# Performance work log

Measured on AMD Instinct MI355X. Metric: run time of the kernel, lower is better.

The kernel has to match this reference:

```python
import jax, jax.numpy as jnp
import numpy as np

N, E, IN_DIM, OUT_DIM = 50000, 800000, 128, 128
NEG_SLOPE = 0.01  # F.leaky_relu default


def gcn_conv(x, W, b, src, dst, n_nodes):
    """PyG GCNConv: symmetric norm with self-loops, linear (no bias) -> aggregate -> +bias.
    Self-loop contribution added analytically (norm = deg_inv_sqrt[i]^2) instead of
    materializing an extended edge list."""
    h = x @ W.T  # [N, out]
    deg = jnp.zeros((n_nodes,), x.dtype).at[dst].add(1.0) + 1.0  # in-degree incl. self-loop
    dis = jax.lax.rsqrt(deg)  # deg^{-1/2}
    norm = dis[src] * dis[dst]  # [E]
    msgs = h[src] * norm[:, None]  # gather + scale, [E, out]
    agg = jax.ops.segment_sum(msgs, dst, num_segments=n_nodes)  # scatter-add
    agg = agg + h * (dis * dis)[:, None]  # self-loop messages
    return agg + b


def setup_inputs() -> dict:
    key = jax.random.key(0)
    ks = jax.random.split(key, 6)
    x = jax.random.normal(ks[0], (N, IN_DIM), jnp.float32)
    edge_index = jax.random.randint(ks[1], (2, E), 0, N, dtype=jnp.int32)
    batch = jnp.zeros((N,), jnp.int32)
    W1 = jax.random.normal(ks[2], (OUT_DIM, IN_DIM), jnp.float32) * (1.0 / np.sqrt(IN_DIM))
    b1 = jnp.zeros((OUT_DIM,), jnp.float32)
    W2 = jax.random.normal(ks[3], (OUT_DIM, OUT_DIM), jnp.float32) * (1.0 / np.sqrt(OUT_DIM))
    b2 = jnp.zeros((OUT_DIM,), jnp.float32)
    return {"x": x, "edge_index": edge_index, "batch": batch,
            "W1": W1, "b1": b1, "W2": W2, "b2": b2}


def reference(x, edge_index, batch, W1, b1, W2, b2):
    src, dst = edge_index[0], edge_index[1]
    n = x.shape[0]
    h = gcn_conv(x, W1, b1, src, dst, n)
    h = jax.nn.leaky_relu(h, NEG_SLOPE)
    # dropout is identity in eval mode (training=False)
    return gcn_conv(h, W2, b2, src, dst, n)
```

## Files before the change

### kernel.cpp

```cpp
#include <hip/hip_runtime.h>
#include <hip/hip_bf16.h>
#include <hip/hip_fp16.h>

#define DIM 128
#define NCHUNK 256
#define XLD 136
#define WLD 136

typedef unsigned short u16;
typedef unsigned int u32;
typedef __attribute__((ext_vector_type(8))) short bf16x8;
typedef __attribute__((ext_vector_type(4))) float f32x4;

__device__ __forceinline__ float bfbits2f(u16 u) {
    return __uint_as_float(((u32)u) << 16);
}
__device__ __forceinline__ u16 f2bf(float f) {
    __hip_bfloat16 b = __float2bfloat16(f);
    return *reinterpret_cast<u16*>(&b);
}
__device__ __forceinline__ u32 pack2bf(float lo, float hi) {
    return (u32)f2bf(lo) | ((u32)f2bf(hi) << 16);
}
__device__ __forceinline__ float h16tof(u16 u) {
    __half hh = *reinterpret_cast<__half*>(&u);
    return __half2float(hh);
}
__device__ __forceinline__ u16 ftoh16(float f) {
    __half hh = __float2half(f);
    return *reinterpret_cast<u16*>(&hh);
}

__global__ void k_probe(const u16* __restrict__ x, int* __restrict__ flagp) {
    if (threadIdx.x == 0 && blockIdx.x == 0) {
        int weird = 0;
        for (int i = 0; i < 256; i += 2) {
            u16 v = x[i];
            int e = (v >> 7) & 0xff;
            if ((v & 0x7fff) != 0 && (e >= 133 || e <= 100)) weird++;
        }
        *flagp = (weird > 16) ? 1 : 0;
    }
}

__global__ __launch_bounds__(256) void k_count(const int* __restrict__ dst,
                                               int* __restrict__ counts,
                                               int* __restrict__ rank, int E) {
    int e = blockIdx.x * blockDim.x + threadIdx.x;
    if (e < E) rank[e] = atomicAdd(&counts[dst[e]], 1);
}

__global__ __launch_bounds__(256) void k_chunksum(const int* __restrict__ counts,
                                                  int* __restrict__ chunksum,
                                                  int N, int chunk) {
    __shared__ int r[256];
    int t = threadIdx.x, b = blockIdx.x;
    int idx = b * chunk + t;
    r[t] = (t < chunk && idx < N) ? counts[idx] : 0;
    __syncthreads();
    for (int off = 128; off > 0; off >>= 1) {
        if (t < off) r[t] += r[t + off];
        __syncthreads();
    }
    if (t == 0) chunksum[b] = r[0];
}

__global__ void k_scanbase(const int* __restrict__ chunksum,
                           int* __restrict__ chunkbase,
                           int* __restrict__ rowptr, int N) {
    if (threadIdx.x == 0 && blockIdx.x == 0) {
        int run = 0;
        for (int i = 0; i < NCHUNK; ++i) { chunkbase[i] = run; run += chunksum[i]; }
        rowptr[N] = run;
    }
}

__global__ __launch_bounds__(256) void k_rowptr(const int* __restrict__ counts,
                                                const int* __restrict__ chunkbase,
                                                int* __restrict__ rowptr,
                                                float* __restrict__ dis,
                                                u32* __restrict__ pay,
                                                int N, int chunk) {
    __shared__ int sc[256];
    int t = threadIdx.x, b = blockIdx.x;
    int idx = b * chunk + t;
    int v = (t < chunk && idx < N) ? counts[idx] : 0;
    sc[t] = v;
    __syncthreads();
    for (int off = 1; off < 256; off <<= 1) {
        int add = (t >= off) ? sc[t - off] : 0;
        __syncthreads();
        sc[t] += add;
        __syncthreads();
    }
    if (t < chunk && idx < N) {
        rowptr[idx] = chunkbase[b] + sc[t] - v;
        float dv = rsqrtf((float)v + 1.0f);
        dis[idx] = dv;
        pay[idx] = ((u32)idx << 16) | (u32)ftoh16(dv);
    }
}

__global__ __launch_bounds__(256) void k_fill(const int* __restrict__ src,
                                              const int* __restrict__ dst,
                                              const int* __restrict__ rowptr,
                                              const int* __restrict__ rank,
                                              const u32* __restrict__ pay,
                                              u32* __restrict__ elist, int E) {
    int e = blockIdx.x * blockDim.x + threadIdx.x;
    if (e < E) {
        int d = dst[e];
        int s = src[e];
        elist[rowptr[d] + rank[e]] = pay[s];
    }
}

__global__ __launch_bounds__(256) void k_gemm(const void* __restrict__ in,
                                              const void* __restrict__ W,
                                              u16* __restrict__ h, int N,
                                              const int* __restrict__ flagp, int in_mode) {
    __shared__ u16 Xs[64 * XLD];
    __shared__ u16 Wsh[128 * WLD];
    const int tid = threadIdx.x;
    const int flag = *flagp;
    const int in_f32 = in_mode ? flag : 0;
    const int n0 = blockIdx.x * 64;

    if (flag) {
        const float* Wf = (const float*)W;
        for (int t = tid; t < 128 * 32; t += 256) {
            int r = t >> 5, c4 = (t & 31) * 4;
            float4 w = *(const float4*)(Wf + r * DIM + c4);
            uint2 pw = make_uint2(pack2bf(w.x, w.y), pack2bf(w.z, w.w));
            *(uint2*)(Wsh + r * WLD + c4) = pw;
        }
    } else {
        const u16* Wu = (const u16*)W;
        for (int t = tid; t < 128 * 16; t += 256) {
            int r = t >> 4, c8 = (t & 15) * 8;
            *(int4*)(Wsh + r * WLD + c8) = *(const int4*)(Wu + r * DIM + c8);
        }
    }
    if (in_f32) {
        const float* xf = (const float*)in;
        for (int t = tid; t < 64 * 32; t += 256) {
            int r = t >> 5, c4 = (t & 31) * 4;
            int n = n0 + r;
            float4 xv = make_float4(0.f, 0.f, 0.f, 0.f);
            if (n < N) xv = *(const float4*)(xf + (size_t)n * DIM + c4);
            uint2 px = make_uint2(pack2bf(xv.x, xv.y), pack2bf(xv.z, xv.w));
            *(uint2*)(Xs + r * XLD + c4) = px;
        }
    } else {
        const u16* xu = (const u16*)in;
        for (int t = tid; t < 64 * 16; t += 256) {
            int r = t >> 4, c8 = (t & 15) * 8;
            int n = n0 + r;
            int4 v = make_int4(0, 0, 0, 0);
            if (n < N) v = *(const int4*)(xu + (size_t)n * DIM + c8);
            *(int4*)(Xs + r * XLD + c8) = v;
        }
    }
    __syncthreads();

    const int wid = tid >> 6;
    const int lane = tid & 63;
    const int m_base = wid * 16;
    const int idx16 = lane & 15;
    const int koff = (lane >> 4) * 8;

    bf16x8 afrag[4];
#pragma unroll
    for (int ks = 0; ks < 4; ++ks)
        afrag[ks] = *(const bf16x8*)(Xs + (m_base + idx16) * XLD + ks * 32 + koff);

    f32x4 acc[8];
#pragma unroll
    for (int ct = 0; ct < 8; ++ct) acc[ct] = (f32x4){0.f, 0.f, 0.f, 0.f};

#pragma unroll
    for (int ct = 0; ct < 8; ++ct) {
#pragma unroll
        for (int ks = 0; ks < 4; ++ks) {
            bf16x8 bfrag = *(const bf16x8*)(Wsh + (ct * 16 + idx16) * WLD + ks * 32 + koff);
            acc[ct] = __builtin_amdgcn_mfma_f32_16x16x32_bf16(afrag[ks], bfrag, acc[ct], 0, 0, 0);
        }
    }

    const int drow = (lane >> 4) * 4;
#pragma unroll
    for (int ct = 0; ct < 8; ++ct) {
#pragma unroll
        for (int r = 0; r < 4; ++r) {
            int row = n0 + m_base + drow + r;
            if (row < N) h[(size_t)row * DIM + ct * 16 + idx16] = f2bf(acc[ct][r]);
        }
    }
}

template <bool RELU, bool OUT_BF16>
__global__ __launch_bounds__(256) void k_agg(const u16* __restrict__ h,
                                             const float* __restrict__ dis,
                                             const int* __restrict__ rowptr,
                                             const u32* __restrict__ elist,
                                             const void* __restrict__ bias,
                                             void* __restrict__ out, int N,
                                             const int* __restrict__ flagp) {
    const int lane = threadIdx.x & 63;
    const int d = blockIdx.x * 4 + (threadIdx.x >> 6);
    if (d >= N) return;
    const int flag = *flagp;

    const int start = rowptr[d];
    const int end = rowptr[d + 1];
    const float dd = dis[d];

    float accA[8], accB[8];
#pragma unroll
    for (int k = 0; k < 8; ++k) { accA[k] = 0.f; accB[k] = 0.f; }

    int j = start;
    for (; j + 8 <= end; j += 8) {
        u32 ev[8];
#pragma unroll
        for (int k = 0; k < 8; ++k) ev[k] = elist[j + k];
        u32 hv[8];
#pragma unroll
        for (int k = 0; k < 8; ++k)
            hv[k] = *(const u32*)(h + ((size_t)(ev[k] >> 16)) * DIM + lane * 2);
#pragma unroll
        for (int k = 0; k < 8; ++k) {
            float w = h16tof((u16)(ev[k] & 0xffff));
            accA[k] = fmaf(bfbits2f((u16)(hv[k] & 0xffff)), w, accA[k]);
            accB[k] = fmaf(bfbits2f((u16)(hv[k] >> 16)), w, accB[k]);
        }
    }
    for (; j < end; ++j) {
        u32 e0 = elist[j];
        float w0 = h16tof((u16)(e0 & 0xffff));
        u32 u0 = *(const u32*)(h + ((size_t)(e0 >> 16)) * DIM + lane * 2);
        accA[0] = fmaf(bfbits2f((u16)(u0 & 0xffff)), w0, accA[0]);
        accB[0] = fmaf(bfbits2f((u16)(u0 >> 16)), w0, accB[0]);
    }
    float acc0 = ((accA[0] + accA[1]) + (accA[2] + accA[3])) +
                 ((accA[4] + accA[5]) + (accA[6] + accA[7]));
    float acc1 = ((accB[0] + accB[1]) + (accB[2] + accB[3])) +
                 ((accB[4] + accB[5]) + (accB[6] + accB[7]));
    acc0 *= dd;
    acc1 *= dd;
    {
        float d2 = dd * dd;
        u32 u = *(const u32*)(h + (size_t)d * DIM + lane * 2);
        acc0 = fmaf(bfbits2f((u16)(u & 0xffff)), d2, acc0);
        acc1 = fmaf(bfbits2f((u16)(u >> 16)), d2, acc1);
    }
    int c = lane * 2;
    float b0, b1;
    if (flag) {
        b0 = ((const float*)bias)[c];
        b1 = ((const float*)bias)[c + 1];
    } else {
        b0 = bfbits2f(((const u16*)bias)[c]);
        b1 = bfbits2f(((const u16*)bias)[c + 1]);
    }
    acc0 += b0;
    acc1 += b1;
    if (RELU) {
        acc0 = acc0 > 0.f ? acc0 : 0.01f * acc0;
        acc1 = acc1 > 0.f ? acc1 : 0.01f * acc1;
    }
    if (OUT_BF16) {
        u32 packed = (u32)f2bf(acc0) | ((u32)f2bf(acc1) << 16);
        *(u32*)((u16*)out + (size_t)d * DIM + c) = packed;
    } else {
        *(float2*)((float*)out + (size_t)d * DIM + c) = make_float2(acc0, acc1);
    }
}

extern "C" void kernel_launch(void* const* d_in, const int* in_sizes, int n_in,
                              void* d_out, int out_size, void* d_ws, size_t ws_size,
                              hipStream_t stream) {
    const void* x  = d_in[0];
    const int*  ei = (const int*)d_in[1];
    const void* W1 = d_in[3];
    const void* b1 = d_in[4];
    const void* W2 = d_in[5];
    const void* b2 = d_in[6];

    const int N = in_sizes[0] / DIM;
    const int E = in_sizes[1] / 2;
    const int* src = ei;
    const int* dst = ei + E;
    const int chunk = (N + NCHUNK - 1) / NCHUNK;

    char* ws = (char*)d_ws;
    size_t o = 0;
    int*   flagp    = (int*)(ws + o);   o += 256;
    float* dis      = (float*)(ws + o); o += (((size_t)N * 4 + 255) & ~(size_t)255);
    int*   counts   = (int*)(ws + o);   o += (((size_t)N * 4 + 255) & ~(size_t)255);
    int*   rowptr   = (int*)(ws + o);   o += (((size_t)(N + 1) * 4 + 255) & ~(size_t)255);
    u32*   pay      = (u32*)(ws + o);   o += (((size_t)N * 4 + 255) & ~(size_t)255);
    int*   chunksum = (int*)(ws + o);   o += 1024;
    int*   chunkbase= (int*)(ws + o);   o += 1024;
    int*   rank     = (int*)(ws + o);   o += (((size_t)E * 4 + 255) & ~(size_t)255);
    u32*   elist    = (u32*)(ws + o);   o += (((size_t)E * 4 + 255) & ~(size_t)255);
    u16*   h        = (u16*)(ws + o);

    const int eblk = (E + 255) / 256;
    const int gblk = (N + 63) / 64;
    const int ablk = (N + 3) / 4;

    k_probe<<<1, 64, 0, stream>>>((const u16*)x, flagp);
    hipMemsetAsync(counts, 0, (size_t)N * 4, stream);
    k_count<<<eblk, 256, 0, stream>>>(dst, counts, rank, E);
    k_chunksum<<<NCHUNK, 256, 0, stream>>>(counts, chunksum, N, chunk);
    k_scanbase<<<1, 64, 0, stream>>>(chunksum, chunkbase, rowptr, N);
    k_rowptr<<<NCHUNK, 256, 0, stream>>>(counts, chunkbase, rowptr, dis, pay, N, chunk);
    k_fill<<<eblk, 256, 0, stream>>>(src, dst, rowptr, rank, pay, elist, E);

    u16* act = (u16*)d_out;

    k_gemm<<<gblk, 256, 0, stream>>>(x, W1, h, N, flagp, 1);
    k_agg<true, true><<<ablk, 256, 0, stream>>>(h, dis, rowptr, elist, b1, act, N, flagp);

    k_gemm<<<gblk, 256, 0, stream>>>(act, W2, h, N, flagp, 0);
    k_agg<false, false><<<ablk, 256, 0, stream>>>(h, dis, rowptr, elist, b2, d_out, N, flagp);
}
```

Baseline: 267.5 us.

## Fuse CSR construction into one cooperative kernel with grid syncs

Replaces the probe, memset, count, chunk-sum, scan-base, rowptr and fill launches with a single cooperative kernel that separates phases with grid.sync(). The serial single-thread chunk-base scan is replaced by a per-block reduction over the preceding chunk sums. The aim is to remove launch overhead and the gaps between six small dependent kernels. In exchange it relies on a fixed grid of 1024 blocks being co-resident for cooperative launch, and it pays for the grid-wide barriers.

```diff
diff --git a/kernel.cpp b/kernel.cpp
--- a/kernel.cpp
+++ b/kernel.cpp
@@ -1,6 +1,9 @@
 #include <hip/hip_runtime.h>
 #include <hip/hip_bf16.h>
 #include <hip/hip_fp16.h>
+#include <hip/hip_cooperative_groups.h>
+
+namespace cg = cooperative_groups;
 
 #define DIM 128
 #define NCHUNK 256
@@ -31,8 +34,28 @@
     return *reinterpret_cast<u16*>(&hh);
 }
 
-__global__ void k_probe(const u16* __restrict__ x, int* __restrict__ flagp) {
-    if (threadIdx.x == 0 && blockIdx.x == 0) {
+__global__ __launch_bounds__(256) void k_csr(const u16* __restrict__ x,
+                                             const int* __restrict__ src,
+                                             const int* __restrict__ dst,
+                                             int* __restrict__ counts,
+                                             int* __restrict__ rank,
+                                             int* __restrict__ chunksum,
+                                             int* __restrict__ rowptr,
+                                             float* __restrict__ dis,
+                                             u32* __restrict__ pay,
+                                             u32* __restrict__ elist,
+                                             int* __restrict__ flagp,
+                                             int N, int E, int chunk) {
+    cg::grid_group grid = cg::this_grid();
+    const int tid = threadIdx.x;
+    const int gtid = blockIdx.x * 256 + tid;
+    const int gsize = gridDim.x * 256;
+
+    __shared__ int red[256];
+    __shared__ int sc[256];
+
+    for (int i = gtid; i < N; i += gsize) counts[i] = 0;
+    if (gtid == 0) {
         int weird = 0;
         for (int i = 0; i < 256; i += 2) {
             u16 v = x[i];
@@ -41,78 +64,55 @@
         }
         *flagp = (weird > 16) ? 1 : 0;
     }
-}
-
-__global__ __launch_bounds__(256) void k_count(const int* __restrict__ dst,
-                                               int* __restrict__ counts,
-                                               int* __restrict__ rank, int E) {
-    int e = blockIdx.x * blockDim.x + threadIdx.x;
-    if (e < E) rank[e] = atomicAdd(&counts[dst[e]], 1);
-}
-
-__global__ __launch_bounds__(256) void k_chunksum(const int* __restrict__ counts,
-                                                  int* __restrict__ chunksum,
-                                                  int N, int chunk) {
-    __shared__ int r[256];
-    int t = threadIdx.x, b = blockIdx.x;
-    int idx = b * chunk + t;
-    r[t] = (t < chunk && idx < N) ? counts[idx] : 0;
-    __syncthreads();
-    for (int off = 128; off > 0; off >>= 1) {
-        if (t < off) r[t] += r[t + off];
-        __syncthreads();
-    }
-    if (t == 0) chunksum[b] = r[0];
-}
-
-__global__ void k_scanbase(const int* __restrict__ chunksum,
-                           int* __restrict__ chunkbase,
-                           int* __restrict__ rowptr, int N) {
-    if (threadIdx.x == 0 && blockIdx.x == 0) {
-        int run = 0;
-        for (int i = 0; i < NCHUNK; ++i) { chunkbase[i] = run; run += chunksum[i]; }
-        rowptr[N] = run;
-    }
-}
-
-__global__ __launch_bounds__(256) void k_rowptr(const int* __restrict__ counts,
-                                                const int* __restrict__ chunkbase,
-                                                int* __restrict__ rowptr,
-                                                float* __restrict__ dis,
-                                                u32* __restrict__ pay,
-                                                int N, int chunk) {
-    __shared__ int sc[256];
-    int t = threadIdx.x, b = blockIdx.x;
-    int idx = b * chunk + t;
-    int v = (t < chunk && idx < N) ? counts[idx] : 0;
-    sc[t] = v;
-    __syncthreads();
-    for (int off = 1; off < 256; off <<= 1) {
-        int add = (t >= off) ? sc[t - off] : 0;
-        __syncthreads();
-        sc[t] += add;
-        __syncthreads();
-    }
-    if (t < chunk && idx < N) {
-        rowptr[idx] = chunkbase[b] + sc[t] - v;
-        float dv = rsqrtf((float)v + 1.0f);
-        dis[idx] = dv;
-        pay[idx] = ((u32)idx << 16) | (u32)ftoh16(dv);
-    }
-}
-
-__global__ __launch_bounds__(256) void k_fill(const int* __restrict__ src,
-                                              const int* __restrict__ dst,
-                                              const int* __restrict__ rowptr,
-                                              const int* __restrict__ rank,
-                                              const u32* __restrict__ pay,
-                                              u32* __restrict__ elist, int E) {
-    int e = blockIdx.x * blockDim.x + threadIdx.x;
-    if (e < E) {
-        int d = dst[e];
-        int s = src[e];
-        elist[rowptr[d] + rank[e]] = pay[s];
-    }
+    grid.sync();
+
+    for (int e = gtid; e < E; e += gsize) rank[e] = atomicAdd(&counts[dst[e]], 1);
+    grid.sync();
+
+    for (int cb = blockIdx.x; cb < NCHUNK; cb += gridDim.x) {
+        int idx = cb * chunk + tid;
+        red[tid] = (tid < chunk && idx < N) ? counts[idx] : 0;
+        __syncthreads();
+        for (int off = 128; off > 0; off >>= 1) {
+            if (tid < off) red[tid] += red[tid + off];
+            __syncthreads();
+        }
+        if (tid == 0) chunksum[cb] = red[0];
+        __syncthreads();
+    }
+    grid.sync();
+
+    for (int cb = blockIdx.x; cb < NCHUNK; cb += gridDim.x) {
+        red[tid] = (tid < cb) ? chunksum[tid] : 0;
+        __syncthreads();
+        for (int off = 128; off > 0; off >>= 1) {
+            if (tid < off) red[tid] += red[tid + off];
+            __syncthreads();
+        }
+        int base = red[0];
+        int idx = cb * chunk + tid;
+        int v = (tid < chunk && idx < N) ? counts[idx] : 0;
+        sc[tid] = v;
+        __syncthreads();
+        for (int off = 1; off < 256; off <<= 1) {
+            int add = (tid >= off) ? sc[tid - off] : 0;
+            __syncthreads();
+            sc[tid] += add;
+            __syncthreads();
+        }
+        if (tid < chunk && idx < N) {
+            rowptr[idx] = base + sc[tid] - v;
+            float dv = rsqrtf((float)v + 1.0f);
+            dis[idx] = dv;
+            pay[idx] = ((u32)idx << 16) | (u32)ftoh16(dv);
+        }
+        if (cb == NCHUNK - 1 && tid == 0) rowptr[N] = base + sc[255];
+        __syncthreads();
+    }
+    grid.sync();
+
+    for (int e = gtid; e < E; e += gsize)
+        elist[rowptr[dst[e]] + rank[e]] = pay[src[e]];
 }
 
 __global__ __launch_bounds__(256) void k_gemm(const void* __restrict__ in,
@@ -280,8 +280,8 @@
 extern "C" void kernel_launch(void* const* d_in, const int* in_sizes, int n_in,
                               void* d_out, int out_size, void* d_ws, size_t ws_size,
                               hipStream_t stream) {
-    const void* x  = d_in[0];
-    const int*  ei = (const int*)d_in[1];
+    const u16* x  = (const u16*)d_in[0];
+    const int* ei = (const int*)d_in[1];
     const void* W1 = d_in[3];
     const void* b1 = d_in[4];
     const void* W2 = d_in[5];
@@ -301,22 +301,22 @@
     int*   rowptr   = (int*)(ws + o);   o += (((size_t)(N + 1) * 4 + 255) & ~(size_t)255);
     u32*   pay      = (u32*)(ws + o);   o += (((size_t)N * 4 + 255) & ~(size_t)255);
     int*   chunksum = (int*)(ws + o);   o += 1024;
-    int*   chunkbase= (int*)(ws + o);   o += 1024;
     int*   rank     = (int*)(ws + o);   o += (((size_t)E * 4 + 255) & ~(size_t)255);
     u32*   elist    = (u32*)(ws + o);   o += (((size_t)E * 4 + 255) & ~(size_t)255);
     u16*   h        = (u16*)(ws + o);
 
-    const int eblk = (E + 255) / 256;
     const int gblk = (N + 63) / 64;
     const int ablk = (N + 3) / 4;
 
-    k_probe<<<1, 64, 0, stream>>>((const u16*)x, flagp);
-    hipMemsetAsync(counts, 0, (size_t)N * 4, stream);
-    k_count<<<eblk, 256, 0, stream>>>(dst, counts, rank, E);
-    k_chunksum<<<NCHUNK, 256, 0, stream>>>(counts, chunksum, N, chunk);
-    k_scanbase<<<1, 64, 0, stream>>>(chunksum, chunkbase, rowptr, N);
-    k_rowptr<<<NCHUNK, 256, 0, stream>>>(counts, chunkbase, rowptr, dis, pay, N, chunk);
-    k_fill<<<eblk, 256, 0, stream>>>(src, dst, rowptr, rank, pay, elist, E);
+    {
+        void* args[] = {
+            (void*)&x, (void*)&src, (void*)&dst, (void*)&counts, (void*)&rank,
+            (void*)&chunksum, (void*)&rowptr, (void*)&dis, (void*)&pay,
+            (void*)&elist, (void*)&flagp, (void*)&N, (void*)&E, (void*)&chunk
+        };
+        hipLaunchCooperativeKernel((const void*)k_csr, dim3(1024), dim3(256),
+                                   args, 0, stream);
+    }
 
     u16* act = (u16*)d_out;
 
```

After: 637.9 us. 138% more time.
